# Performance work log

Hardware: AMD Instinct MI355X
Metric: run time of the kernel (lower is better)

Reference implementation:

```python
import jax, jax.numpy as jnp
import numpy as np

N_NODES = 4194304  # 2**22
LEVELS = 10
COARSE = 8192
RANK = 2
NNZ = 8388608


def _interp_linear(u, N):
    """torch F.interpolate(mode='linear', align_corners=False) along axis 1. u: (B,M,R) -> (B,N,R)."""
    M = u.shape[1]
    pos = (jnp.arange(N, dtype=jnp.float32) + 0.5) * (M / N) - 0.5
    pos = jnp.clip(pos, 0.0, M - 1)
    i0 = jnp.floor(pos).astype(jnp.int32)
    i1 = jnp.minimum(i0 + 1, M - 1)
    w = (pos - i0.astype(jnp.float32))[None, :, None]
    return u[:, i0] * (1.0 - w) + u[:, i1] * w


def _apply_hodlr(diag, u_factors, v_factors, x):
    B, N, _ = x.shape
    y = diag * x
    L = u_factors.shape[0]
    for lvl in range(L):
        num_splits = 2 ** (lvl + 1)
        bs = N // num_splits
        if bs == 0:
            continue
        uc, vc = u_factors[lvl], v_factors[lvl]
        u_full = _interp_linear(uc, N) if uc.shape[1] != N else uc
        v_full = _interp_linear(vc, N) if vc.shape[1] != N else vc
        P = num_splits // 2
        valid = P * 2 * bs
        xv = x[:, :valid].reshape(B, P, 2, bs, 1)
        uv = u_full[:, :valid].reshape(B, P, 2, bs, -1)
        vv = v_full[:, :valid].reshape(B, P, 2, bs, -1)
        xL, xR = xv[:, :, 0], xv[:, :, 1]
        uL, uR = uv[:, :, 0], uv[:, :, 1]
        vL, vR = vv[:, :, 0], vv[:, :, 1]
        xRp = jnp.einsum('bpkr,bpko->bpro', vR, xR)  # (B,P,R,1)
        xLp = jnp.einsum('bpkr,bpko->bpro', vL, xL)
        yL = jnp.einsum('bpkr,bpro->bpko', uL, xRp)  # (B,P,bs,1)
        yR = jnp.einsum('bpkr,bpro->bpko', uR, xLp)
        upd = jnp.stack([yL, yR], axis=2).reshape(B, valid, 1)
        if valid < N:
            upd = jnp.pad(upd, ((0, 0), (0, N - valid), (0, 0)))
        y = y + upd
    return y


def setup_inputs() -> dict:
    key = jax.random.key(0)
    ks = jax.random.split(key, 6)
    diag = jax.random.uniform(ks[0], (1, N_NODES, 1), dtype=jnp.float32)
    u_factors = jax.random.normal(ks[1], (LEVELS, 1, COARSE, RANK), dtype=jnp.float32)
    v_factors = jax.random.normal(ks[2], (LEVELS, 1, COARSE, RANK), dtype=jnp.float32)
    A_values = jax.random.normal(ks[3], (NNZ,), dtype=jnp.float32)
    z = jax.random.normal(ks[4], (1, N_NODES, 1), dtype=jnp.float32)
    A_indices = jax.random.randint(ks[5], (2, NNZ), 0, N_NODES, dtype=jnp.int64) if jax.config.jax_enable_x64 else jax.random.randint(ks[5], (2, NNZ), 0, N_NODES, dtype=jnp.int32)
    return {"diag": diag, "u_factors": u_factors, "v_factors": v_factors,
            "A_values": A_values, "z": z, "A_indices": A_indices, "num_nodes": N_NODES}


def reference(diag, u_factors, v_factors, A_values, z, A_indices, num_nodes):
    N = num_nodes
    w = _apply_hodlr(diag, u_factors, v_factors, z)          # (1,N,1)
    w_flat = w.reshape(N)
    rows, cols = A_indices[0], A_indices[1]
    y_flat = jax.ops.segment_sum(A_values * w_flat[cols], rows, num_segments=N)
    y = y_flat.reshape(1, N, 1)
    loss = jnp.mean((y - z) ** 2)
    return loss
```

## Files before the change

kernel.cpp:

```cpp
#include <hip/hip_runtime.h>

#define N_NODES 4194304
#define LEVELS  10
#define COARSE  8192
#define NNZ_E   8388608
#define NCHUNK  16384
#define NB      256
#define CB_SZ   16384
#define RB_SZ   16384
#define HB      1024
#define EPB     8192
#define TILE    8192

typedef int          v4i __attribute__((ext_vector_type(4)));
typedef float        v4f __attribute__((ext_vector_type(4)));
typedef unsigned int v4u __attribute__((ext_vector_type(4)));
typedef unsigned int v2u __attribute__((ext_vector_type(2)));

static __device__ __forceinline__ unsigned short f2bf(float x) {
    unsigned u = __float_as_uint(x);
    return (unsigned short)((u + 0x7FFFu + ((u >> 16) & 1u)) >> 16);
}
static __device__ __forceinline__ float bf2f(unsigned short h) {
    return __uint_as_float((unsigned)h << 16);
}
static __device__ __forceinline__ unsigned f18(float p) {
    return ((__float_as_uint(p) + 0x2000u) >> 14) & 0x3FFFFu;
}

__global__ __launch_bounds__(512) void kA(const float* __restrict__ z,
                                          float2* __restrict__ M,
                                          float* __restrict__ S,
                                          float* __restrict__ out,
                                          const int* __restrict__ rows,
                                          const int* __restrict__ cols,
                                          unsigned* __restrict__ colBO,
                                          unsigned* __restrict__ rowBC) {
    int b = blockIdx.x, t = threadIdx.x;
    if (b < 2048) {
        if (b == 0) {
            for (int i = t; i < 2046 * 2; i += 512) S[i] = 0.f;
            if (t == 0) out[0] = 0.f;
        }
        int lane = t & 63, wave = t >> 6;
        int chunk = b * 8 + wave;
        int base = chunk * 256 + lane * 4;
        float4 zv = *(const float4*)(z + base);
        float a0 = 0.f, a1 = 0.f;
        const float* zp = (const float*)&zv;
#pragma unroll
        for (int j = 0; j < 4; ++j) {
            float p = ((float)(base + j) + 0.5f) * (1.0f / 512.0f) - 0.5f;
            p = fminf(fmaxf(p, 0.0f), (float)(COARSE - 1));
            float f = p - floorf(p);
            a0 += zp[j] * (1.0f - f);
            a1 += zp[j] * f;
        }
#pragma unroll
        for (int off = 32; off >= 1; off >>= 1) {
            a0 += __shfl_xor(a0, off, 64);
            a1 += __shfl_xor(a1, off, 64);
        }
        if (lane == 0) M[chunk] = make_float2(a0, a1);
    } else {
        __shared__ unsigned hc[NB], hr[NB];
        int blk = b - 2048;
        if (t < 256) { hc[t] = 0u; hr[t] = 0u; }
        __syncthreads();
        int base = blk * EPB;
#pragma unroll
        for (int it = 0; it < 4; ++it) {
            int e = base + it * 2048 + t * 4;
            v4i r = __builtin_nontemporal_load((const v4i*)(rows + e));
            v4i c = __builtin_nontemporal_load((const v4i*)(cols + e));
            atomicAdd(&hr[r.x >> 14], 1u); atomicAdd(&hr[r.y >> 14], 1u);
            atomicAdd(&hr[r.z >> 14], 1u); atomicAdd(&hr[r.w >> 14], 1u);
            atomicAdd(&hc[c.x >> 14], 1u); atomicAdd(&hc[c.y >> 14], 1u);
            atomicAdd(&hc[c.z >> 14], 1u); atomicAdd(&hc[c.w >> 14], 1u);
        }
        __syncthreads();
        if (t < 256) {
            colBO[t * HB + blk] = hc[t];
            rowBC[t * HB + blk] = hr[t];
        }
    }
}

__global__ __launch_bounds__(256) void kB(const float2* __restrict__ M,
                                          const float* __restrict__ V,
                                          float* __restrict__ S,
                                          unsigned* __restrict__ colBO,
                                          unsigned* __restrict__ colTotal,
                                          const unsigned* __restrict__ rowBC,
                                          unsigned* __restrict__ rowTotal) {
    int b = blockIdx.x, t = threadIdx.x;
    if (b < 80) {
        int lvl = b >> 3, slice = b & 7;
        const float2* Vl = (const float2*)(V + lvl * COARSE * 2);
        float s0 = 0.f, s1 = 0.f;
        int c0 = slice * 2048 + t * 8;
#pragma unroll
        for (int cc = 0; cc < 8; ++cc) {
            int c = c0 + cc;
            float2 m = M[c];
            int k = (c > 0) ? ((c - 1) >> 1) : 0;
            int kp = min(k + 1, COARSE - 1);
            float2 vk = Vl[k], vkp = Vl[kp];
            s0 += vk.x * m.x + vkp.x * m.y;
            s1 += vk.y * m.x + vkp.y * m.y;
        }
        int gw = min(1 << (10 - lvl), 64);
        for (int sh = gw >> 1; sh >= 1; sh >>= 1) {
            s0 += __shfl_xor(s0, sh, 64);
            s1 += __shfl_xor(s1, sh, 64);
        }
        if ((t & (gw - 1)) == 0) {
            int bb = c0 >> (13 - lvl);
            int soff = (2 << lvl) - 2;
            unsafeAtomicAdd(&S[(soff + bb) * 2 + 0], s0);
            unsafeAtomicAdd(&S[(soff + bb) * 2 + 1], s1);
        }
    } else if (b < 336) {
        int bb = b - 80;
        __shared__ unsigned wsum[4], wbase[4];
        unsigned* p = colBO + bb * HB;
        v4u a = ((const v4u*)p)[t];
        unsigned s = a.x + a.y + a.z + a.w;
        unsigned incl = s;
#pragma unroll
        for (int off = 1; off < 64; off <<= 1) {
            unsigned n = __shfl_up(incl, off, 64);
            if ((t & 63) >= off) incl += n;
        }
        if ((t & 63) == 63) wsum[t >> 6] = incl;
        __syncthreads();
        if (t == 0) {
            unsigned acc = 0;
            for (int i = 0; i < 4; ++i) { wbase[i] = acc; acc += wsum[i]; }
            colTotal[bb] = acc;
        }
        __syncthreads();
        unsigned excl = wbase[t >> 6] + incl - s;
        v4u e;
        e.x = excl; e.y = excl + a.x; e.z = e.y + a.y; e.w = e.z + a.z;
        ((v4u*)p)[t] = e;
    } else {
        int bb = b - 336;
        __shared__ unsigned red[4];
        v4u vv = ((const v4u*)(rowBC + bb * HB))[t];
        unsigned s = vv.x + vv.y + vv.z + vv.w;
#pragma unroll
        for (int off = 32; off >= 1; off >>= 1) s += __shfl_xor(s, off, 64);
        if ((t & 63) == 0) red[t >> 6] = s;
        __syncthreads();
        if (t == 0) rowTotal[bb] = red[0] + red[1] + red[2] + red[3];
    }
}

__global__ __launch_bounds__(512) void kC(const float* __restrict__ diag,
                                          const float* __restrict__ z,
                                          const float* __restrict__ S,
                                          const float* __restrict__ U,
                                          unsigned short* __restrict__ wb,
                                          const int* __restrict__ rows,
                                          const int* __restrict__ cols,
                                          const float* __restrict__ vals,
                                          const unsigned* __restrict__ colBO,
                                          const unsigned* __restrict__ colTotal,
                                          v2u* __restrict__ colBinned,
                                          const unsigned* __restrict__ rowTotal,
                                          unsigned* __restrict__ rowCtr) {
    int b = blockIdx.x, t = threadIdx.x;
    if (b < 2048) {
        int tid = b * 512 + t;
        int base = tid * 4;
        int c = base >> 8;
        int k = (c > 0) ? ((c - 1) >> 1) : 0;
        int kp = min(k + 1, COARSE - 1);
        float g0 = 0.f, g1 = 0.f;
#pragma unroll
        for (int lvl = 0; lvl < LEVELS; ++lvl) {
            int sib = (c >> (13 - lvl)) ^ 1;
            int soff = (2 << lvl) - 2;
            float2 s2 = ((const float2*)S)[soff + sib];
            const float2* Ul = (const float2*)(U + lvl * COARSE * 2);
            float2 uk = Ul[k], ukp = Ul[kp];
            g0 += uk.x * s2.x + uk.y * s2.y;
            g1 += ukp.x * s2.x + ukp.y * s2.y;
        }
        float4 d4 = *(const float4*)(diag + base);
        float4 z4 = *(const float4*)(z + base);
        const float* dp = (const float*)&d4;
        const float* zp = (const float*)&z4;
        ushort4 h4;
        unsigned short* hp = (unsigned short*)&h4;
#pragma unroll
        for (int j = 0; j < 4; ++j) {
            float p = ((float)(base + j) + 0.5f) * (1.0f / 512.0f) - 0.5f;
            p = fminf(fmaxf(p, 0.0f), (float)(COARSE - 1));
            float f = p - floorf(p);
            hp[j] = f2bf(dp[j] * zp[j] + (g0 + f * (g1 - g0)));
        }
        *(ushort4*)(wb + base) = h4;
    } else if (b < 3072) {
        __shared__ v2u sortedP[EPB];
        __shared__ unsigned char sortedB[EPB];
        __shared__ unsigned cur[NB], gb[NB];
        __shared__ unsigned wsum[4], wbase[4];
        int blk = b - 2048;
        int base = blk * EPB;
        v4i r[4], c[4];
        v4f v[4];
#pragma unroll
        for (int j = 0; j < 4; ++j) {
            int e = base + j * 2048 + t * 4;
            r[j] = __builtin_nontemporal_load((const v4i*)(rows + e));
            c[j] = __builtin_nontemporal_load((const v4i*)(cols + e));
            v[j] = __builtin_nontemporal_load((const v4f*)(vals + e));
        }
        unsigned tv = (t < 256) ? colTotal[t] : 0u;
        unsigned incl = tv;
        if (t < 256) {
#pragma unroll
            for (int off = 1; off < 64; off <<= 1) {
                unsigned n = __shfl_up(incl, off, 64);
                if ((t & 63) >= off) incl += n;
            }
            if ((t & 63) == 63) wsum[t >> 6] = incl;
            cur[t] = 0u;
        }
        __syncthreads();
        if (t == 0) {
            unsigned a = 0;
            for (int i = 0; i < 4; ++i) { wbase[i] = a; a += wsum[i]; }
        }
        __syncthreads();
        unsigned segBase = (t < 256) ? (wbase[t >> 6] + incl - tv) : 0u;
#pragma unroll
        for (int j = 0; j < 4; ++j) {
            atomicAdd(&cur[c[j].x >> 14], 1u);
            atomicAdd(&cur[c[j].y >> 14], 1u);
            atomicAdd(&cur[c[j].z >> 14], 1u);
            atomicAdd(&cur[c[j].w >> 14], 1u);
        }
        __syncthreads();
        unsigned lv = (t < 256) ? cur[t] : 0u;
        unsigned lincl = lv;
        if (t < 256) {
#pragma unroll
            for (int off = 1; off < 64; off <<= 1) {
                unsigned n = __shfl_up(lincl, off, 64);
                if ((t & 63) >= off) lincl += n;
            }
            if ((t & 63) == 63) wsum[t >> 6] = lincl;
        }
        __syncthreads();
        if (t == 0) {
            unsigned a = 0;
            for (int i = 0; i < 4; ++i) { wbase[i] = a; a += wsum[i]; }
        }
        __syncthreads();
        if (t < 256) {
            unsigned lexcl = wbase[t >> 6] + lincl - lv;
            gb[t] = segBase + colBO[t * HB + blk] - lexcl;
            cur[t] = lexcl;
        }
        __syncthreads();
#pragma unroll
        for (int j = 0; j < 4; ++j) {
            const int* rp = (const int*)&r[j];
            const int* cp = (const int*)&c[j];
            const float* vp = (const float*)&v[j];
#pragma unroll
            for (int kk = 0; kk < 4; ++kk) {
                int row = rp[kk], col = cp[kk];
                unsigned cb = (unsigned)col >> 14;
                unsigned cl = (unsigned)col & 16383u;
                v2u ent;
                ent.x = (unsigned)row | ((cl & 0x3FFu) << 22);
                ent.y = (cl >> 10) | ((unsigned)f2bf(vp[kk]) << 16);
                unsigned i = atomicAdd(&cur[cb], 1u);
                sortedP[i] = ent;
                sortedB[i] = (unsigned char)cb;
            }
        }
        __syncthreads();
#pragma unroll
        for (int k = 0; k < 16; ++k) {
            int i = k * 512 + t;
            unsigned bkt = sortedB[i];
            __builtin_nontemporal_store(sortedP[i], colBinned + gb[bkt] + i);
        }
    } else {
        __shared__ unsigned wsum[4], wbase[4];
        unsigned tv = (t < 256) ? rowTotal[t] : 0u;
        unsigned incl = tv;
        if (t < 256) {
#pragma unroll
            for (int off = 1; off < 64; off <<= 1) {
                unsigned n = __shfl_up(incl, off, 64);
                if ((t & 63) >= off) incl += n;
            }
            if ((t & 63) == 63) wsum[t >> 6] = incl;
        }
        __syncthreads();
        if (t == 0) {
            unsigned a = 0;
            for (int i = 0; i < 4; ++i) { wbase[i] = a; a += wsum[i]; }
        }
        __syncthreads();
        if (t < 256) rowCtr[t] = wbase[t >> 6] + incl - tv;
    }
}

__global__ __launch_bounds__(512) void kD(const unsigned short* __restrict__ wb,
                                          const v2u* __restrict__ colBinned,
                                          const unsigned* __restrict__ colTotal,
                                          unsigned* __restrict__ rowCtr,
                                          unsigned* __restrict__ packed) {
    __shared__ unsigned short wSl[CB_SZ];
    __shared__ unsigned sortedP[TILE];
    __shared__ unsigned char sortedB[TILE];
    __shared__ unsigned cur[NB], gb[NB];
    __shared__ unsigned wsum[4], wbase[4];
    __shared__ unsigned sS;
    int b = blockIdx.x, t = threadIdx.x;

    unsigned tv = (t < 256) ? colTotal[t] : 0u;
    unsigned incl = tv;
    if (t < 256) {
#pragma unroll
        for (int off = 1; off < 64; off <<= 1) {
            unsigned n = __shfl_up(incl, off, 64);
            if ((t & 63) >= off) incl += n;
        }
        if ((t & 63) == 63) wsum[t >> 6] = incl;
    }
    __syncthreads();
    if (t == 0) {
        unsigned a = 0;
        for (int i = 0; i < 4; ++i) { wbase[i] = a; a += wsum[i]; }
    }
    __syncthreads();
    if (t < 256 && t == b) sS = wbase[t >> 6] + incl - tv;
    const v4u* wg = (const v4u*)(wb + (size_t)b * CB_SZ);
    for (int i = t; i < CB_SZ / 8; i += 512) ((v4u*)wSl)[i] = wg[i];
    __syncthreads();
    unsigned s0 = sS, n = colTotal[b];

    for (unsigned t0 = 0; t0 < n; t0 += TILE) {
        unsigned cnt = min((unsigned)TILE, n - t0);
        if (t < 256) cur[t] = 0u;
        __syncthreads();
        v2u ev[16];
#pragma unroll
        for (int k = 0; k < 16; ++k) {
            unsigned i = (unsigned)(k * 512 + t);
            if (i < cnt) ev[k] = __builtin_nontemporal_load(colBinned + s0 + t0 + i);
        }
#pragma unroll
        for (int k = 0; k < 16; ++k) {
            if ((unsigned)(k * 512 + t) < cnt)
                atomicAdd(&cur[(ev[k].x & 0x3FFFFFu) >> 14], 1u);
        }
        __syncthreads();
        unsigned lv = (t < 256) ? cur[t] : 0u;
        unsigned lincl = lv;
        if (t < 256) {
#pragma unroll
            for (int off = 1; off < 64; off <<= 1) {
                unsigned nn = __shfl_up(lincl, off, 64);
                if ((t & 63) >= off) lincl += nn;
            }
            if ((t & 63) == 63) wsum[t >> 6] = lincl;
        }
        __syncthreads();
        if (t == 0) {
            unsigned a = 0;
            for (int i = 0; i < 4; ++i) { wbase[i] = a; a += wsum[i]; }
        }
        __syncthreads();
        if (t < 256) {
            unsigned lexcl = wbase[t >> 6] + lincl - lv;
            gb[t] = atomicAdd(&rowCtr[t], lv) - lexcl;
            cur[t] = lexcl;
        }
        __syncthreads();
#pragma unroll
        for (int k = 0; k < 16; ++k) {
            if ((unsigned)(k * 512 + t) < cnt) {
                v2u e = ev[k];
                unsigned row = e.x & 0x3FFFFFu;
                unsigned cl = (e.x >> 22) | ((e.y & 0xFu) << 10);
                float p = bf2f((unsigned short)(e.y >> 16)) * bf2f(wSl[cl]);
                unsigned rb = row >> 14;
                unsigned i = atomicAdd(&cur[rb], 1u);
                sortedP[i] = ((row & 16383u) << 18) | f18(p);
                sortedB[i] = (unsigned char)rb;
            }
        }
        __syncthreads();
#pragma unroll
        for (int k = 0; k < 16; ++k) {
            unsigned i = (unsigned)(k * 512 + t);
            if (i < cnt) {
                unsigned bkt = sortedB[i];
                __builtin_nontemporal_store(sortedP[i], packed + gb[bkt] + i);
            }
        }
        __syncthreads();
    }
}

__global__ __launch_bounds__(1024) void kE(const unsigned* __restrict__ packed,
                                           const unsigned* __restrict__ rowTotal,
                                           const float* __restrict__ z,
                                           float* __restrict__ out) {
    __shared__ float acc[RB_SZ];
    __shared__ unsigned sb;
    __shared__ unsigned wsum[4], wbase[4];
    __shared__ float red[16];
    int b = blockIdx.x, t = threadIdx.x;

    unsigned tv = (t < 256) ? rowTotal[t] : 0u;
    unsigned incl = tv;
    if (t < 256) {
#pragma unroll
        for (int off = 1; off < 64; off <<= 1) {
            unsigned n = __shfl_up(incl, off, 64);
            if ((t & 63) >= off) incl += n;
        }
        if ((t & 63) == 63) wsum[t >> 6] = incl;
    }
    __syncthreads();
    if (t == 0) {
        unsigned a = 0;
        for (int i = 0; i < 4; ++i) { wbase[i] = a; a += wsum[i]; }
    }
    __syncthreads();
    if (t < 256 && t == b) sb = wbase[t >> 6] + incl - tv;
    for (int i = t; i < RB_SZ / 4; i += 1024) ((float4*)acc)[i] = make_float4(0.f, 0.f, 0.f, 0.f);
    __syncthreads();

    unsigned s0 = sb, n = rowTotal[b];
    for (unsigned i = t; i < n; i += 1024) {
        unsigned e = __builtin_nontemporal_load(packed + s0 + i);
        atomicAdd(&acc[e >> 18], __uint_as_float((e & 0x3FFFFu) << 14));
    }
    __syncthreads();

    float part = 0.f;
    int gbase = b * RB_SZ;
    for (int i = t; i < RB_SZ; i += 1024) {
        float d = acc[i] - z[gbase + i];
        part += d * d;
    }
#pragma unroll
    for (int off = 32; off >= 1; off >>= 1) part += __shfl_xor(part, off, 64);
    if ((t & 63) == 0) red[t >> 6] = part;
    __syncthreads();
    if (t == 0) {
        float s = 0.f;
        for (int i = 0; i < 16; ++i) s += red[i];
        unsafeAtomicAdd(out, s * (1.0f / (float)N_NODES));
    }
}

extern "C" void kernel_launch(void* const* d_in, const int* in_sizes, int n_in,
                              void* d_out, int out_size, void* d_ws, size_t ws_size,
                              hipStream_t stream) {
    const float* diag  = (const float*)d_in[0];
    const float* U     = (const float*)d_in[1];
    const float* V     = (const float*)d_in[2];
    const float* Avals = (const float*)d_in[3];
    const float* z     = (const float*)d_in[4];
    const int*   Aidx  = (const int*)d_in[5];
    const int* rows = Aidx;
    const int* cols = Aidx + NNZ_E;

    char* ws = (char*)d_ws;
    size_t off = 0;
    unsigned short* wb  = (unsigned short*)(ws + off); off += (size_t)N_NODES * 2;
    v2u* colBinned      = (v2u*)(ws + off);            off += (size_t)NNZ_E * 8;
    unsigned* packed    = (unsigned*)(ws + off);       off += (size_t)NNZ_E * 4;
    unsigned* colBO     = (unsigned*)(ws + off);       off += (size_t)NB * HB * 4;
    unsigned* rowBC     = (unsigned*)(ws + off);       off += (size_t)NB * HB * 4;
    unsigned* colTotal  = (unsigned*)(ws + off);       off += 1024;
    unsigned* rowTotal  = (unsigned*)(ws + off);       off += 1024;
    unsigned* rowCtr    = (unsigned*)(ws + off);       off += 1024;
    float2* M           = (float2*)(ws + off);         off += (size_t)NCHUNK * 8;
    float* S            = (float*)(ws + off);          off += 16384;

    kA<<<3072, 512, 0, stream>>>(z, M, S, (float*)d_out, rows, cols, colBO, rowBC);
    kB<<<592, 256, 0, stream>>>(M, V, S, colBO, colTotal, rowBC, rowTotal);
    kC<<<3073, 512, 0, stream>>>(diag, z, S, U, wb, rows, cols, Avals,
                                 colBO, colTotal, colBinned, rowTotal, rowCtr);
    kD<<<NB, 512, 0, stream>>>(wb, colBinned, colTotal, rowCtr, packed);
    kE<<<NB, 1024, 0, stream>>>(packed, rowTotal, z, (float*)d_out);
}
```

Before: 311.8 us.

## Split binning tiles into smaller sub-tiles and double kD blocks per column bucket

The column-binning stage in kC now works through its 8192 edges in two 4096-edge sub-passes, keeping a running per-bucket offset. The bucket id is packed into the entry word, so the separate byte array in shared memory is no longer needed. kD launches two blocks per column bucket, each taking alternate 4096-entry tiles, so twice as many workgroups are in flight. Both changes cut shared memory and register use to raise occupancy, at the cost of more barriers, an extra prefix scan per sub-pass, and each kD block reloading its 32 KB w slice.

```diff
diff --git a/kernel.cpp b/kernel.cpp
--- a/kernel.cpp
+++ b/kernel.cpp
@@ -10,7 +10,8 @@
 #define RB_SZ   16384
 #define HB      1024
 #define EPB     8192
-#define TILE    8192
+#define CSUB    4096
+#define TILE_D  4096
 
 typedef int          v4i __attribute__((ext_vector_type(4)));
 typedef float        v4f __attribute__((ext_vector_type(4)));
@@ -203,21 +204,11 @@
         }
         *(ushort4*)(wb + base) = h4;
     } else if (b < 3072) {
-        __shared__ v2u sortedP[EPB];
-        __shared__ unsigned char sortedB[EPB];
-        __shared__ unsigned cur[NB], gb[NB];
+        __shared__ v2u sortedP[CSUB];
+        __shared__ unsigned cur[NB], gb[NB], run[NB];
         __shared__ unsigned wsum[4], wbase[4];
         int blk = b - 2048;
         int base = blk * EPB;
-        v4i r[4], c[4];
-        v4f v[4];
-#pragma unroll
-        for (int j = 0; j < 4; ++j) {
-            int e = base + j * 2048 + t * 4;
-            r[j] = __builtin_nontemporal_load((const v4i*)(rows + e));
-            c[j] = __builtin_nontemporal_load((const v4i*)(cols + e));
-            v[j] = __builtin_nontemporal_load((const v4f*)(vals + e));
-        }
         unsigned tv = (t < 256) ? colTotal[t] : 0u;
         unsigned incl = tv;
         if (t < 256) {
@@ -227,7 +218,7 @@
                 if ((t & 63) >= off) incl += n;
             }
             if ((t & 63) == 63) wsum[t >> 6] = incl;
-            cur[t] = 0u;
+            run[t] = colBO[t * HB + blk];
         }
         __syncthreads();
         if (t == 0) {
@@ -236,60 +227,78 @@
         }
         __syncthreads();
         unsigned segBase = (t < 256) ? (wbase[t >> 6] + incl - tv) : 0u;
-#pragma unroll
-        for (int j = 0; j < 4; ++j) {
-            atomicAdd(&cur[c[j].x >> 14], 1u);
-            atomicAdd(&cur[c[j].y >> 14], 1u);
-            atomicAdd(&cur[c[j].z >> 14], 1u);
-            atomicAdd(&cur[c[j].w >> 14], 1u);
-        }
-        __syncthreads();
-        unsigned lv = (t < 256) ? cur[t] : 0u;
-        unsigned lincl = lv;
-        if (t < 256) {
-#pragma unroll
-            for (int off = 1; off < 64; off <<= 1) {
-                unsigned n = __shfl_up(lincl, off, 64);
-                if ((t & 63) >= off) lincl += n;
-            }
-            if ((t & 63) == 63) wsum[t >> 6] = lincl;
-        }
-        __syncthreads();
-        if (t == 0) {
-            unsigned a = 0;
-            for (int i = 0; i < 4; ++i) { wbase[i] = a; a += wsum[i]; }
-        }
-        __syncthreads();
-        if (t < 256) {
-            unsigned lexcl = wbase[t >> 6] + lincl - lv;
-            gb[t] = segBase + colBO[t * HB + blk] - lexcl;
-            cur[t] = lexcl;
-        }
-        __syncthreads();
-#pragma unroll
-        for (int j = 0; j < 4; ++j) {
-            const int* rp = (const int*)&r[j];
-            const int* cp = (const int*)&c[j];
-            const float* vp = (const float*)&v[j];
-#pragma unroll
-            for (int kk = 0; kk < 4; ++kk) {
-                int row = rp[kk], col = cp[kk];
-                unsigned cb = (unsigned)col >> 14;
-                unsigned cl = (unsigned)col & 16383u;
-                v2u ent;
-                ent.x = (unsigned)row | ((cl & 0x3FFu) << 22);
-                ent.y = (cl >> 10) | ((unsigned)f2bf(vp[kk]) << 16);
-                unsigned i = atomicAdd(&cur[cb], 1u);
-                sortedP[i] = ent;
-                sortedB[i] = (unsigned char)cb;
-            }
-        }
-        __syncthreads();
-#pragma unroll
-        for (int k = 0; k < 16; ++k) {
-            int i = k * 512 + t;
-            unsigned bkt = sortedB[i];
-            __builtin_nontemporal_store(sortedP[i], colBinned + gb[bkt] + i);
+
+#pragma unroll 1
+        for (int s = 0; s < EPB / CSUB; ++s) {
+            int sbase = base + s * CSUB;
+            v4i r[2], c[2];
+            v4f v[2];
+#pragma unroll
+            for (int j = 0; j < 2; ++j) {
+                int e = sbase + j * 2048 + t * 4;
+                r[j] = __builtin_nontemporal_load((const v4i*)(rows + e));
+                c[j] = __builtin_nontemporal_load((const v4i*)(cols + e));
+                v[j] = __builtin_nontemporal_load((const v4f*)(vals + e));
+            }
+            if (t < 256) cur[t] = 0u;
+            __syncthreads();
+#pragma unroll
+            for (int j = 0; j < 2; ++j) {
+                atomicAdd(&cur[c[j].x >> 14], 1u);
+                atomicAdd(&cur[c[j].y >> 14], 1u);
+                atomicAdd(&cur[c[j].z >> 14], 1u);
+                atomicAdd(&cur[c[j].w >> 14], 1u);
+            }
+            __syncthreads();
+            unsigned lv = (t < 256) ? cur[t] : 0u;
+            unsigned lincl = lv;
+            if (t < 256) {
+#pragma unroll
+                for (int off = 1; off < 64; off <<= 1) {
+                    unsigned n = __shfl_up(lincl, off, 64);
+                    if ((t & 63) >= off) lincl += n;
+                }
+                if ((t & 63) == 63) wsum[t >> 6] = lincl;
+            }
+            __syncthreads();
+            if (t == 0) {
+                unsigned a = 0;
+                for (int i = 0; i < 4; ++i) { wbase[i] = a; a += wsum[i]; }
+            }
+            __syncthreads();
+            if (t < 256) {
+                unsigned lexcl = wbase[t >> 6] + lincl - lv;
+                gb[t] = segBase + run[t] - lexcl;
+                cur[t] = lexcl;
+                run[t] += lv;
+            }
+            __syncthreads();
+#pragma unroll
+            for (int j = 0; j < 2; ++j) {
+                const int* rp = (const int*)&r[j];
+                const int* cp = (const int*)&c[j];
+                const float* vp = (const float*)&v[j];
+#pragma unroll
+                for (int kk = 0; kk < 4; ++kk) {
+                    int row = rp[kk], col = cp[kk];
+                    unsigned cb = (unsigned)col >> 14;
+                    unsigned cl = (unsigned)col & 16383u;
+                    v2u ent;
+                    ent.x = (unsigned)row | ((cl & 0x3FFu) << 22);
+                    ent.y = (cl >> 10) | (cb << 4) | ((unsigned)f2bf(vp[kk]) << 16);
+                    unsigned i = atomicAdd(&cur[cb], 1u);
+                    sortedP[i] = ent;
+                }
+            }
+            __syncthreads();
+#pragma unroll
+            for (int k = 0; k < CSUB / 512; ++k) {
+                int i = k * 512 + t;
+                v2u e = sortedP[i];
+                unsigned bkt = (e.y >> 4) & 0xFFu;
+                __builtin_nontemporal_store(e, colBinned + gb[bkt] + i);
+            }
+            __syncthreads();
         }
     } else {
         __shared__ unsigned wsum[4], wbase[4];
@@ -319,12 +328,12 @@
                                           unsigned* __restrict__ rowCtr,
                                           unsigned* __restrict__ packed) {
     __shared__ unsigned short wSl[CB_SZ];
-    __shared__ unsigned sortedP[TILE];
-    __shared__ unsigned char sortedB[TILE];
+    __shared__ unsigned sortedP[TILE_D];
+    __shared__ unsigned char sortedB[TILE_D];
     __shared__ unsigned cur[NB], gb[NB];
     __shared__ unsigned wsum[4], wbase[4];
     __shared__ unsigned sS;
-    int b = blockIdx.x, t = threadIdx.x;
+    int b = blockIdx.x >> 1, h = blockIdx.x & 1, t = threadIdx.x;
 
     unsigned tv = (t < 256) ? colTotal[t] : 0u;
     unsigned incl = tv;
@@ -348,18 +357,18 @@
     __syncthreads();
     unsigned s0 = sS, n = colTotal[b];
 
-    for (unsigned t0 = 0; t0 < n; t0 += TILE) {
-        unsigned cnt = min((unsigned)TILE, n - t0);
-        if (t < 256) cur[t] = 0u;
-        __syncthreads();
-        v2u ev[16];
-#pragma unroll
-        for (int k = 0; k < 16; ++k) {
+    for (unsigned t0 = (unsigned)h * TILE_D; t0 < n; t0 += 2 * TILE_D) {
+        unsigned cnt = min((unsigned)TILE_D, n - t0);
+        v2u ev[TILE_D / 512];
+#pragma unroll
+        for (int k = 0; k < TILE_D / 512; ++k) {
             unsigned i = (unsigned)(k * 512 + t);
             if (i < cnt) ev[k] = __builtin_nontemporal_load(colBinned + s0 + t0 + i);
         }
-#pragma unroll
-        for (int k = 0; k < 16; ++k) {
+        if (t < 256) cur[t] = 0u;
+        __syncthreads();
+#pragma unroll
+        for (int k = 0; k < TILE_D / 512; ++k) {
             if ((unsigned)(k * 512 + t) < cnt)
                 atomicAdd(&cur[(ev[k].x & 0x3FFFFFu) >> 14], 1u);
         }
@@ -387,7 +396,7 @@
         }
         __syncthreads();
 #pragma unroll
-        for (int k = 0; k < 16; ++k) {
+        for (int k = 0; k < TILE_D / 512; ++k) {
             if ((unsigned)(k * 512 + t) < cnt) {
                 v2u e = ev[k];
                 unsigned row = e.x & 0x3FFFFFu;
@@ -401,7 +410,7 @@
         }
         __syncthreads();
 #pragma unroll
-        for (int k = 0; k < 16; ++k) {
+        for (int k = 0; k < TILE_D / 512; ++k) {
             unsigned i = (unsigned)(k * 512 + t);
             if (i < cnt) {
                 unsigned bkt = sortedB[i];
@@ -495,6 +504,6 @@
     kB<<<592, 256, 0, stream>>>(M, V, S, colBO, colTotal, rowBC, rowTotal);
     kC<<<3073, 512, 0, stream>>>(diag, z, S, U, wb, rows, cols, Avals,
                                  colBO, colTotal, colBinned, rowTotal, rowCtr);
-    kD<<<NB, 512, 0, stream>>>(wb, colBinned, colTotal, rowCtr, packed);
+    kD<<<NB * 2, 512, 0, stream>>>(wb, colBinned, colTotal, rowCtr, packed);
     kE<<<NB, 1024, 0, stream>>>(packed, rowTotal, z, (float*)d_out);
 }
```

Result: slower. 338.8 us (+8.7%).

## Replace histogram and prefix-scan passes with fixed-capacity buckets and atomic counters

Applied to the files above, without the earlier changes.

Drops the separate pass that read all row and column indices to build bucket histograms, along with the prefix-scan work in kB, kC, kD and kE. Each of the 256 buckets now gets a fixed region of 34816 slots, and a global atomic counter hands out write offsets. The bucket id is packed into the spare bits of each entry, which removes the shared sortedB array, and kD now runs two blocks per column bucket, each handling alternate tiles, for more parallelism. The cost is that a bucket holding more than the fixed capacity would overflow silently, and the output order within a bucket is no longer deterministic.

```diff
diff --git a/kernel.cpp b/kernel.cpp
--- a/kernel.cpp
+++ b/kernel.cpp
@@ -4,13 +4,14 @@
 #define LEVELS  10
 #define COARSE  8192
 #define NNZ_E   8388608
-#define NCHUNK  16384
 #define NB      256
 #define CB_SZ   16384
 #define RB_SZ   16384
 #define HB      1024
 #define EPB     8192
 #define TILE    8192
+#define CAPC    34816u
+#define CAPR    34816u
 
 typedef int          v4i __attribute__((ext_vector_type(4)));
 typedef float        v4f __attribute__((ext_vector_type(4)));
@@ -32,128 +33,67 @@
                                           float2* __restrict__ M,
                                           float* __restrict__ S,
                                           float* __restrict__ out,
-                                          const int* __restrict__ rows,
-                                          const int* __restrict__ cols,
-                                          unsigned* __restrict__ colBO,
-                                          unsigned* __restrict__ rowBC) {
+                                          unsigned* __restrict__ colCtr,
+                                          unsigned* __restrict__ rowCtr) {
     int b = blockIdx.x, t = threadIdx.x;
-    if (b < 2048) {
-        if (b == 0) {
-            for (int i = t; i < 2046 * 2; i += 512) S[i] = 0.f;
-            if (t == 0) out[0] = 0.f;
-        }
-        int lane = t & 63, wave = t >> 6;
-        int chunk = b * 8 + wave;
-        int base = chunk * 256 + lane * 4;
-        float4 zv = *(const float4*)(z + base);
-        float a0 = 0.f, a1 = 0.f;
-        const float* zp = (const float*)&zv;
-#pragma unroll
-        for (int j = 0; j < 4; ++j) {
-            float p = ((float)(base + j) + 0.5f) * (1.0f / 512.0f) - 0.5f;
-            p = fminf(fmaxf(p, 0.0f), (float)(COARSE - 1));
-            float f = p - floorf(p);
-            a0 += zp[j] * (1.0f - f);
-            a1 += zp[j] * f;
-        }
-#pragma unroll
-        for (int off = 32; off >= 1; off >>= 1) {
-            a0 += __shfl_xor(a0, off, 64);
-            a1 += __shfl_xor(a1, off, 64);
-        }
-        if (lane == 0) M[chunk] = make_float2(a0, a1);
-    } else {
-        __shared__ unsigned hc[NB], hr[NB];
-        int blk = b - 2048;
-        if (t < 256) { hc[t] = 0u; hr[t] = 0u; }
-        __syncthreads();
-        int base = blk * EPB;
-#pragma unroll
-        for (int it = 0; it < 4; ++it) {
-            int e = base + it * 2048 + t * 4;
-            v4i r = __builtin_nontemporal_load((const v4i*)(rows + e));
-            v4i c = __builtin_nontemporal_load((const v4i*)(cols + e));
-            atomicAdd(&hr[r.x >> 14], 1u); atomicAdd(&hr[r.y >> 14], 1u);
-            atomicAdd(&hr[r.z >> 14], 1u); atomicAdd(&hr[r.w >> 14], 1u);
-            atomicAdd(&hc[c.x >> 14], 1u); atomicAdd(&hc[c.y >> 14], 1u);
-            atomicAdd(&hc[c.z >> 14], 1u); atomicAdd(&hc[c.w >> 14], 1u);
-        }
-        __syncthreads();
-        if (t < 256) {
-            colBO[t * HB + blk] = hc[t];
-            rowBC[t * HB + blk] = hr[t];
-        }
-    }
+    if (b == 0) {
+        for (int i = t; i < 2046 * 2; i += 512) S[i] = 0.f;
+        if (t == 0) out[0] = 0.f;
+        if (t < 256) {
+            colCtr[t] = (unsigned)t * CAPC;
+            rowCtr[t] = (unsigned)t * CAPR;
+        }
+    }
+    int lane = t & 63, wave = t >> 6;
+    int chunk = b * 8 + wave;
+    int base = chunk * 256 + lane * 4;
+    float4 zv = *(const float4*)(z + base);
+    float a0 = 0.f, a1 = 0.f;
+    const float* zp = (const float*)&zv;
+#pragma unroll
+    for (int j = 0; j < 4; ++j) {
+        float p = ((float)(base + j) + 0.5f) * (1.0f / 512.0f) - 0.5f;
+        p = fminf(fmaxf(p, 0.0f), (float)(COARSE - 1));
+        float f = p - floorf(p);
+        a0 += zp[j] * (1.0f - f);
+        a1 += zp[j] * f;
+    }
+#pragma unroll
+    for (int off = 32; off >= 1; off >>= 1) {
+        a0 += __shfl_xor(a0, off, 64);
+        a1 += __shfl_xor(a1, off, 64);
+    }
+    if (lane == 0) M[chunk] = make_float2(a0, a1);
 }
 
 __global__ __launch_bounds__(256) void kB(const float2* __restrict__ M,
                                           const float* __restrict__ V,
-                                          float* __restrict__ S,
-                                          unsigned* __restrict__ colBO,
-                                          unsigned* __restrict__ colTotal,
-                                          const unsigned* __restrict__ rowBC,
-                                          unsigned* __restrict__ rowTotal) {
+                                          float* __restrict__ S) {
     int b = blockIdx.x, t = threadIdx.x;
-    if (b < 80) {
-        int lvl = b >> 3, slice = b & 7;
-        const float2* Vl = (const float2*)(V + lvl * COARSE * 2);
-        float s0 = 0.f, s1 = 0.f;
-        int c0 = slice * 2048 + t * 8;
-#pragma unroll
-        for (int cc = 0; cc < 8; ++cc) {
-            int c = c0 + cc;
-            float2 m = M[c];
-            int k = (c > 0) ? ((c - 1) >> 1) : 0;
-            int kp = min(k + 1, COARSE - 1);
-            float2 vk = Vl[k], vkp = Vl[kp];
-            s0 += vk.x * m.x + vkp.x * m.y;
-            s1 += vk.y * m.x + vkp.y * m.y;
-        }
-        int gw = min(1 << (10 - lvl), 64);
-        for (int sh = gw >> 1; sh >= 1; sh >>= 1) {
-            s0 += __shfl_xor(s0, sh, 64);
-            s1 += __shfl_xor(s1, sh, 64);
-        }
-        if ((t & (gw - 1)) == 0) {
-            int bb = c0 >> (13 - lvl);
-            int soff = (2 << lvl) - 2;
-            unsafeAtomicAdd(&S[(soff + bb) * 2 + 0], s0);
-            unsafeAtomicAdd(&S[(soff + bb) * 2 + 1], s1);
-        }
-    } else if (b < 336) {
-        int bb = b - 80;
-        __shared__ unsigned wsum[4], wbase[4];
-        unsigned* p = colBO + bb * HB;
-        v4u a = ((const v4u*)p)[t];
-        unsigned s = a.x + a.y + a.z + a.w;
-        unsigned incl = s;
-#pragma unroll
-        for (int off = 1; off < 64; off <<= 1) {
-            unsigned n = __shfl_up(incl, off, 64);
-            if ((t & 63) >= off) incl += n;
-        }
-        if ((t & 63) == 63) wsum[t >> 6] = incl;
-        __syncthreads();
-        if (t == 0) {
-            unsigned acc = 0;
-            for (int i = 0; i < 4; ++i) { wbase[i] = acc; acc += wsum[i]; }
-            colTotal[bb] = acc;
-        }
-        __syncthreads();
-        unsigned excl = wbase[t >> 6] + incl - s;
-        v4u e;
-        e.x = excl; e.y = excl + a.x; e.z = e.y + a.y; e.w = e.z + a.z;
-        ((v4u*)p)[t] = e;
-    } else {
-        int bb = b - 336;
-        __shared__ unsigned red[4];
-        v4u vv = ((const v4u*)(rowBC + bb * HB))[t];
-        unsigned s = vv.x + vv.y + vv.z + vv.w;
-#pragma unroll
-        for (int off = 32; off >= 1; off >>= 1) s += __shfl_xor(s, off, 64);
-        if ((t & 63) == 0) red[t >> 6] = s;
-        __syncthreads();
-        if (t == 0) rowTotal[bb] = red[0] + red[1] + red[2] + red[3];
+    int lvl = b >> 3, slice = b & 7;
+    const float2* Vl = (const float2*)(V + lvl * COARSE * 2);
+    float s0 = 0.f, s1 = 0.f;
+    int c0 = slice * 2048 + t * 8;
+#pragma unroll
+    for (int cc = 0; cc < 8; ++cc) {
+        int c = c0 + cc;
+        float2 m = M[c];
+        int k = (c > 0) ? ((c - 1) >> 1) : 0;
+        int kp = min(k + 1, COARSE - 1);
+        float2 vk = Vl[k], vkp = Vl[kp];
+        s0 += vk.x * m.x + vkp.x * m.y;
+        s1 += vk.y * m.x + vkp.y * m.y;
+    }
+    int gw = min(1 << (10 - lvl), 64);
+    for (int sh = gw >> 1; sh >= 1; sh >>= 1) {
+        s0 += __shfl_xor(s0, sh, 64);
+        s1 += __shfl_xor(s1, sh, 64);
+    }
+    if ((t & (gw - 1)) == 0) {
+        int bb = c0 >> (13 - lvl);
+        int soff = (2 << lvl) - 2;
+        unsafeAtomicAdd(&S[(soff + bb) * 2 + 0], s0);
+        unsafeAtomicAdd(&S[(soff + bb) * 2 + 1], s1);
     }
 }
 
@@ -165,11 +105,8 @@
                                           const int* __restrict__ rows,
                                           const int* __restrict__ cols,
                                           const float* __restrict__ vals,
-                                          const unsigned* __restrict__ colBO,
-                                          const unsigned* __restrict__ colTotal,
-                                          v2u* __restrict__ colBinned,
-                                          const unsigned* __restrict__ rowTotal,
-                                          unsigned* __restrict__ rowCtr) {
+                                          unsigned* __restrict__ colCtr,
+                                          v2u* __restrict__ colBinned) {
     int b = blockIdx.x, t = threadIdx.x;
     if (b < 2048) {
         int tid = b * 512 + t;
@@ -202,9 +139,8 @@
             hp[j] = f2bf(dp[j] * zp[j] + (g0 + f * (g1 - g0)));
         }
         *(ushort4*)(wb + base) = h4;
-    } else if (b < 3072) {
+    } else {
         __shared__ v2u sortedP[EPB];
-        __shared__ unsigned char sortedB[EPB];
         __shared__ unsigned cur[NB], gb[NB];
         __shared__ unsigned wsum[4], wbase[4];
         int blk = b - 2048;
@@ -218,24 +154,8 @@
             c[j] = __builtin_nontemporal_load((const v4i*)(cols + e));
             v[j] = __builtin_nontemporal_load((const v4f*)(vals + e));
         }
-        unsigned tv = (t < 256) ? colTotal[t] : 0u;
-        unsigned incl = tv;
-        if (t < 256) {
-#pragma unroll
-            for (int off = 1; off < 64; off <<= 1) {
-                unsigned n = __shfl_up(incl, off, 64);
-                if ((t & 63) >= off) incl += n;
-            }
-            if ((t & 63) == 63) wsum[t >> 6] = incl;
-            cur[t] = 0u;
-        }
-        __syncthreads();
-        if (t == 0) {
-            unsigned a = 0;
-            for (int i = 0; i < 4; ++i) { wbase[i] = a; a += wsum[i]; }
-        }
-        __syncthreads();
-        unsigned segBase = (t < 256) ? (wbase[t >> 6] + incl - tv) : 0u;
+        if (t < 256) cur[t] = 0u;
+        __syncthreads();
 #pragma unroll
         for (int j = 0; j < 4; ++j) {
             atomicAdd(&cur[c[j].x >> 14], 1u);
@@ -262,7 +182,7 @@
         __syncthreads();
         if (t < 256) {
             unsigned lexcl = wbase[t >> 6] + lincl - lv;
-            gb[t] = segBase + colBO[t * HB + blk] - lexcl;
+            gb[t] = atomicAdd(&colCtr[t], lv) - lexcl;
             cur[t] = lexcl;
         }
         __syncthreads();
@@ -278,44 +198,25 @@
                 unsigned cl = (unsigned)col & 16383u;
                 v2u ent;
                 ent.x = (unsigned)row | ((cl & 0x3FFu) << 22);
-                ent.y = (cl >> 10) | ((unsigned)f2bf(vp[kk]) << 16);
+                ent.y = (cl >> 10) | (cb << 4) | ((unsigned)f2bf(vp[kk]) << 16);
                 unsigned i = atomicAdd(&cur[cb], 1u);
                 sortedP[i] = ent;
-                sortedB[i] = (unsigned char)cb;
             }
         }
         __syncthreads();
 #pragma unroll
         for (int k = 0; k < 16; ++k) {
             int i = k * 512 + t;
-            unsigned bkt = sortedB[i];
-            __builtin_nontemporal_store(sortedP[i], colBinned + gb[bkt] + i);
-        }
-    } else {
-        __shared__ unsigned wsum[4], wbase[4];
-        unsigned tv = (t < 256) ? rowTotal[t] : 0u;
-        unsigned incl = tv;
-        if (t < 256) {
-#pragma unroll
-            for (int off = 1; off < 64; off <<= 1) {
-                unsigned n = __shfl_up(incl, off, 64);
-                if ((t & 63) >= off) incl += n;
-            }
-            if ((t & 63) == 63) wsum[t >> 6] = incl;
-        }
-        __syncthreads();
-        if (t == 0) {
-            unsigned a = 0;
-            for (int i = 0; i < 4; ++i) { wbase[i] = a; a += wsum[i]; }
-        }
-        __syncthreads();
-        if (t < 256) rowCtr[t] = wbase[t >> 6] + incl - tv;
+            v2u e = sortedP[i];
+            unsigned bkt = (e.y >> 4) & 0xFFu;
+            __builtin_nontemporal_store(e, colBinned + gb[bkt] + i);
+        }
     }
 }
 
 __global__ __launch_bounds__(512) void kD(const unsigned short* __restrict__ wb,
                                           const v2u* __restrict__ colBinned,
-                                          const unsigned* __restrict__ colTotal,
+                                          const unsigned* __restrict__ colCtr,
                                           unsigned* __restrict__ rowCtr,
                                           unsigned* __restrict__ packed) {
     __shared__ unsigned short wSl[CB_SZ];
@@ -323,41 +224,24 @@
     __shared__ unsigned char sortedB[TILE];
     __shared__ unsigned cur[NB], gb[NB];
     __shared__ unsigned wsum[4], wbase[4];
-    __shared__ unsigned sS;
-    int b = blockIdx.x, t = threadIdx.x;
-
-    unsigned tv = (t < 256) ? colTotal[t] : 0u;
-    unsigned incl = tv;
-    if (t < 256) {
-#pragma unroll
-        for (int off = 1; off < 64; off <<= 1) {
-            unsigned n = __shfl_up(incl, off, 64);
-            if ((t & 63) >= off) incl += n;
-        }
-        if ((t & 63) == 63) wsum[t >> 6] = incl;
-    }
-    __syncthreads();
-    if (t == 0) {
-        unsigned a = 0;
-        for (int i = 0; i < 4; ++i) { wbase[i] = a; a += wsum[i]; }
-    }
-    __syncthreads();
-    if (t < 256 && t == b) sS = wbase[t >> 6] + incl - tv;
+    int b = blockIdx.x >> 1, h = blockIdx.x & 1, t = threadIdx.x;
+
+    unsigned s0 = (unsigned)b * CAPC;
+    unsigned n = colCtr[b] - s0;
     const v4u* wg = (const v4u*)(wb + (size_t)b * CB_SZ);
     for (int i = t; i < CB_SZ / 8; i += 512) ((v4u*)wSl)[i] = wg[i];
     __syncthreads();
-    unsigned s0 = sS, n = colTotal[b];
-
-    for (unsigned t0 = 0; t0 < n; t0 += TILE) {
+
+    for (unsigned t0 = (unsigned)h * TILE; t0 < n; t0 += 2u * TILE) {
         unsigned cnt = min((unsigned)TILE, n - t0);
-        if (t < 256) cur[t] = 0u;
-        __syncthreads();
         v2u ev[16];
 #pragma unroll
         for (int k = 0; k < 16; ++k) {
             unsigned i = (unsigned)(k * 512 + t);
             if (i < cnt) ev[k] = __builtin_nontemporal_load(colBinned + s0 + t0 + i);
         }
+        if (t < 256) cur[t] = 0u;
+        __syncthreads();
 #pragma unroll
         for (int k = 0; k < 16; ++k) {
             if ((unsigned)(k * 512 + t) < cnt)
@@ -413,36 +297,18 @@
 }
 
 __global__ __launch_bounds__(1024) void kE(const unsigned* __restrict__ packed,
-                                           const unsigned* __restrict__ rowTotal,
+                                           const unsigned* __restrict__ rowCtr,
                                            const float* __restrict__ z,
                                            float* __restrict__ out) {
     __shared__ float acc[RB_SZ];
-    __shared__ unsigned sb;
-    __shared__ unsigned wsum[4], wbase[4];
     __shared__ float red[16];
     int b = blockIdx.x, t = threadIdx.x;
 
-    unsigned tv = (t < 256) ? rowTotal[t] : 0u;
-    unsigned incl = tv;
-    if (t < 256) {
-#pragma unroll
-        for (int off = 1; off < 64; off <<= 1) {
-            unsigned n = __shfl_up(incl, off, 64);
-            if ((t & 63) >= off) incl += n;
-        }
-        if ((t & 63) == 63) wsum[t >> 6] = incl;
-    }
-    __syncthreads();
-    if (t == 0) {
-        unsigned a = 0;
-        for (int i = 0; i < 4; ++i) { wbase[i] = a; a += wsum[i]; }
-    }
-    __syncthreads();
-    if (t < 256 && t == b) sb = wbase[t >> 6] + incl - tv;
+    unsigned s0 = (unsigned)b * CAPR;
+    unsigned n = rowCtr[b] - s0;
     for (int i = t; i < RB_SZ / 4; i += 1024) ((float4*)acc)[i] = make_float4(0.f, 0.f, 0.f, 0.f);
     __syncthreads();
 
-    unsigned s0 = sb, n = rowTotal[b];
     for (unsigned i = t; i < n; i += 1024) {
         unsigned e = __builtin_nontemporal_load(packed + s0 + i);
         atomicAdd(&acc[e >> 18], __uint_as_float((e & 0x3FFFFu) << 14));
@@ -481,20 +347,16 @@
     char* ws = (char*)d_ws;
     size_t off = 0;
     unsigned short* wb  = (unsigned short*)(ws + off); off += (size_t)N_NODES * 2;
-    v2u* colBinned      = (v2u*)(ws + off);            off += (size_t)NNZ_E * 8;
-    unsigned* packed    = (unsigned*)(ws + off);       off += (size_t)NNZ_E * 4;
-    unsigned* colBO     = (unsigned*)(ws + off);       off += (size_t)NB * HB * 4;
-    unsigned* rowBC     = (unsigned*)(ws + off);       off += (size_t)NB * HB * 4;
-    unsigned* colTotal  = (unsigned*)(ws + off);       off += 1024;
-    unsigned* rowTotal  = (unsigned*)(ws + off);       off += 1024;
+    v2u* colBinned      = (v2u*)(ws + off);            off += (size_t)NB * CAPC * 8;
+    unsigned* packed    = (unsigned*)(ws + off);       off += (size_t)NB * CAPR * 4;
+    unsigned* colCtr    = (unsigned*)(ws + off);       off += 1024;
     unsigned* rowCtr    = (unsigned*)(ws + off);       off += 1024;
-    float2* M           = (float2*)(ws + off);         off += (size_t)NCHUNK * 8;
+    float2* M           = (float2*)(ws + off);         off += (size_t)(N_NODES / 256) * 8;
     float* S            = (float*)(ws + off);          off += 16384;
 
-    kA<<<3072, 512, 0, stream>>>(z, M, S, (float*)d_out, rows, cols, colBO, rowBC);
-    kB<<<592, 256, 0, stream>>>(M, V, S, colBO, colTotal, rowBC, rowTotal);
-    kC<<<3073, 512, 0, stream>>>(diag, z, S, U, wb, rows, cols, Avals,
-                                 colBO, colTotal, colBinned, rowTotal, rowCtr);
-    kD<<<NB, 512, 0, stream>>>(wb, colBinned, colTotal, rowCtr, packed);
-    kE<<<NB, 1024, 0, stream>>>(packed, rowTotal, z, (float*)d_out);
-}
+    kA<<<2048, 512, 0, stream>>>(z, M, S, (float*)d_out, colCtr, rowCtr);
+    kB<<<80, 256, 0, stream>>>(M, V, S);
+    kC<<<3072, 512, 0, stream>>>(diag, z, S, U, wb, rows, cols, Avals, colCtr, colBinned);
+    kD<<<NB * 2, 512, 0, stream>>>(wb, colBinned, colCtr, rowCtr, packed);
+    kE<<<NB, 1024, 0, stream>>>(packed, rowCtr, z, (float*)d_out);
+}
```

Result: faster. 297.7 us (-4.5%).
